# Kernel optimization log

Hardware: AMD Instinct MI355X
Metric: run time of the kernel (lower is better)

## Reference

```python
import jax, jax.numpy as jnp
import numpy as np

B, T, C = 4, 4096, 512


def setup_inputs() -> dict:
    key = jax.random.key(0)
    ks = jax.random.split(key, 7)
    s = 1.0 / np.sqrt(C)  # ~ torch Linear init scale
    X = jax.random.normal(ks[0], (B, T, C), jnp.float32)
    S_n = jnp.zeros((B, C, C), jnp.float32)
    W_Q = jax.random.normal(ks[1], (C, C), jnp.float32) * s
    b_Q = jax.random.normal(ks[2], (C,), jnp.float32) * s
    W_K = jax.random.normal(ks[3], (C, C), jnp.float32) * s
    b_K = jax.random.normal(ks[4], (C,), jnp.float32) * s
    W_V = jax.random.normal(ks[5], (C, C), jnp.float32) * s
    b_V = jax.random.normal(ks[6], (C,), jnp.float32) * s
    return {"X": X, "S_n": S_n, "W_Q": W_Q, "b_Q": b_Q,
            "W_K": W_K, "b_K": b_K, "W_V": W_V, "b_V": b_V}


def reference(X, S_n, W_Q, b_Q, W_K, b_K, W_V, b_V):
    # forward_chunkwise with chunk_len = 1 (exact simplification):
    #   per step t (gamma g_t from linspace(0.96, 0.99, T)):
    #     inner_t = (q_t . k_t) * v_t            # D = gamma^0 = 1
    #     cross_t = (q_t @ S) * g_t              # e[:,0,:] = g^1
    #     O_t     = tanh(inner_t + cross_t)
    #     S      <- k_t^T v_t + g_t * S          # D[-1] = 1, g**chunk_len = g
    Bx, Tx, Cx = X.shape
    Q = X @ W_Q + b_Q  # [B,T,C]
    K = X @ W_K + b_K
    V = X @ W_V + b_V
    gammas = jnp.linspace(0.96, 0.99, Tx).astype(X.dtype)

    def step(S, inp):
        q, k, v, g = inp  # q,k,v: [B,C]; g: scalar
        inner = jnp.sum(q * k, axis=-1, keepdims=True) * v      # [B,C]
        cross = jnp.einsum('bc,bcd->bd', q, S) * g              # [B,C]
        O = jnp.tanh(inner + cross)
        S_new = jnp.einsum('bc,bd->bcd', k, v) + S * g          # [B,C,C]
        return S_new, O

    # original resets S_n to zeros regardless of the passed-in value
    S0 = jnp.zeros_like(S_n)
    S_final, O = jax.lax.scan(
        step, S0,
        (Q.transpose(1, 0, 2), K.transpose(1, 0, 2), V.transpose(1, 0, 2), gammas))
    out = O.transpose(1, 0, 2)  # [B,T,C]
    return out, S_final
```

## Files before the change

### kernel.cpp

```cpp
#include <hip/hip_runtime.h>
#include <math.h>

#define Bsz  4
#define Tlen 4096
#define Cdim 512
#define CUT  (-12.0f)
#define NBE  8388608

typedef unsigned int u32;
typedef _Float16 f16;
typedef __attribute__((ext_vector_type(8))) _Float16 f16x8;
typedef __attribute__((ext_vector_type(4))) float floatx4;
#define MFMA_F16(a,b,c) __builtin_amdgcn_mfma_f32_16x16x32_f16((a),(b),(c),0,0,0)

union pun8 { uint4 u; f16x8 f; };

__device__ __forceinline__ u32 pack2(f16 a, f16 b) {
    return (u32)__builtin_bit_cast(unsigned short, a) |
           ((u32)__builtin_bit_cast(unsigned short, b) << 16);
}
__device__ __forceinline__ u32 splitpack(float v) {
    f16 h = (f16)v;
    f16 l = (f16)(v - (float)h);
    return pack2(h, l);
}
__device__ __forceinline__ void unpack8(const u32* p, f16x8& h, f16x8& l) {
    uint4 q0 = *(const uint4*)p;
    uint4 q1 = *(const uint4*)(p + 4);
    pun8 ph, pl;
    ph.u.x = __builtin_amdgcn_perm(q0.y, q0.x, 0x05040100u);
    pl.u.x = __builtin_amdgcn_perm(q0.y, q0.x, 0x07060302u);
    ph.u.y = __builtin_amdgcn_perm(q0.w, q0.z, 0x05040100u);
    pl.u.y = __builtin_amdgcn_perm(q0.w, q0.z, 0x07060302u);
    ph.u.z = __builtin_amdgcn_perm(q1.y, q1.x, 0x05040100u);
    pl.u.z = __builtin_amdgcn_perm(q1.y, q1.x, 0x07060302u);
    ph.u.w = __builtin_amdgcn_perm(q1.w, q1.z, 0x05040100u);
    pl.u.w = __builtin_amdgcn_perm(q1.w, q1.z, 0x07060302u);
    h = ph.f; l = pl.f;
}
__device__ __forceinline__ float tanh_fast(float x) {
    return 1.0f - 2.0f / (__expf(2.0f * x) + 1.0f);
}

__global__ __launch_bounds__(256) void prep_kernel(
    const float* __restrict__ X,
    const float* __restrict__ WQ, const float* __restrict__ WK,
    const float* __restrict__ WV,
    f16* __restrict__ Xf, f16* __restrict__ WT,
    float* __restrict__ Lg, float* __restrict__ Wfin, int* __restrict__ sLo) {
    __shared__ char pshm[18432];
    int bid = blockIdx.x, tid = threadIdx.x;
    if (bid < 2048) {
        size_t i = ((size_t)bid * 256 + tid) * 16;
        float v[16];
#pragma unroll
        for (int j = 0; j < 4; ++j) {
            float4 a = *(const float4*)(X + i + j * 4);
            v[j*4+0]=a.x; v[j*4+1]=a.y; v[j*4+2]=a.z; v[j*4+3]=a.w;
        }
        uint4 o0, o1;
        o0.x = pack2((f16)v[0], (f16)v[1]);   o0.y = pack2((f16)v[2], (f16)v[3]);
        o0.z = pack2((f16)v[4], (f16)v[5]);   o0.w = pack2((f16)v[6], (f16)v[7]);
        o1.x = pack2((f16)v[8], (f16)v[9]);   o1.y = pack2((f16)v[10], (f16)v[11]);
        o1.z = pack2((f16)v[12], (f16)v[13]); o1.w = pack2((f16)v[14], (f16)v[15]);
        *(uint4*)(Xf + i) = o0;
        *(uint4*)(Xf + i + 8) = o1;
    } else if (bid < 2240) {
        f16* tile = (f16*)pshm;
        int wb = bid - 2048;
        int mat = wb >> 6, rem = wb & 63;
        int k0 = (rem >> 3) * 64, n0 = (rem & 7) * 64;
        const float* W = (mat == 0) ? WQ : (mat == 1) ? WK : WV;
        int row = tid >> 2, q = tid & 3;
        const float* src = W + (size_t)(k0 + row) * Cdim + n0 + q * 16;
        float vv[16];
#pragma unroll
        for (int j = 0; j < 4; ++j) {
            float4 v = *(const float4*)(src + j * 4);
            vv[j*4+0]=v.x; vv[j*4+1]=v.y; vv[j*4+2]=v.z; vv[j*4+3]=v.w;
        }
#pragma unroll
        for (int j = 0; j < 16; ++j) tile[(q * 16 + j) * 72 + row] = (f16)vv[j];
        __syncthreads();
        f16x8 r0 = *(const f16x8*)(tile + row * 72 + q * 16);
        f16x8 r1 = *(const f16x8*)(tile + row * 72 + q * 16 + 8);
        f16* dst = WT + ((size_t)mat * Cdim + n0 + row) * Cdim + k0 + q * 16;
        *(f16x8*)dst = r0;
        *(f16x8*)(dst + 8) = r1;
    } else {
        float* Lsh = (float*)pshm;
        float* sums = (float*)(pshm + 16400);
        float lg[16];
        float local = 0.f;
        int base = tid * 16;
#pragma unroll
        for (int i = 0; i < 16; ++i) {
            int t = base + i;
            float g = 0.96f + 0.03f * ((float)t * (1.0f / 4095.0f));
            lg[i] = logf(g);
            local += lg[i];
        }
        sums[tid] = local;
        __syncthreads();
        for (int off = 1; off < 256; off <<= 1) {
            float v = sums[tid];
            if (tid >= off) v += sums[tid - off];
            __syncthreads();
            sums[tid] = v;
            __syncthreads();
        }
        float pre = (tid == 0) ? 0.f : sums[tid - 1];
#pragma unroll
        for (int i = 0; i < 16; ++i) {
            Lsh[base + i] = pre;
            pre += lg[i];
        }
        if (tid == 255) Lsh[4096] = pre;
        __syncthreads();
        for (int t = tid; t < 4097; t += 256) Lg[t] = Lsh[t];
        float LT = Lsh[4096];
        for (int s = tid; s < 4096; s += 256) Wfin[s] = __expf(LT - Lsh[s + 1]);
        if (tid < 64) {
            float ref = Lsh[tid * 64 + 1];
            int st_hi = tid >> 1;
            int lo = st_hi;
            for (int st = 0; st < st_hi; ++st)
                if (ref - Lsh[st * 128 + 128] > CUT) { lo = st; break; }
            sLo[tid] = lo;
        }
    }
}

__global__ __launch_bounds__(256, 2) void qkv_mfma(
    const f16* __restrict__ Xf, const f16* __restrict__ WT,
    const float* __restrict__ bQ, const float* __restrict__ bK,
    const float* __restrict__ bV,
    f16* __restrict__ Qf, f16* __restrict__ Kf,
    f16* __restrict__ KT, f16* __restrict__ VT) {
    __shared__ char smem[34816];
    u32* sX = (u32*)smem;
    u32* sW = (u32*)(smem + 16384);
    f16* sB = (f16*)smem;

    int tid = threadIdx.x, lane = tid & 63, wid = tid >> 6;
    int l16 = lane & 15, quad = lane >> 4;
    int wm = wid & 1, wn = wid >> 1;
    int xb = blockIdx.x;
    int mat = xb >> 2, n0 = (xb & 3) * 128;
    int m0 = blockIdx.y * 128;

    floatx4 acc[4][4];
#pragma unroll
    for (int i = 0; i < 4; ++i)
#pragma unroll
        for (int j = 0; j < 4; ++j) acc[i][j] = (floatx4)0.f;

    int srow = tid >> 1, shalf = tid & 1;
    int arow_a = wm * 64 + l16, arow_b = wn * 64 + l16;
    int swz_f = (l16 & 7) << 2;

    for (int kc = 0; kc < Cdim; kc += 64) {
        __syncthreads();
        {
            const f16* gx = Xf + (size_t)(m0 + srow) * Cdim + kc + shalf * 32;
            const f16* gw = WT + ((size_t)(mat * Cdim) + n0 + srow) * Cdim + kc + shalf * 32;
            int wswz = (srow & 7) << 2;
#pragma unroll
            for (int k = 0; k < 4; ++k) {
                uint4 xv = *(const uint4*)(gx + k * 8);
                uint4 wv = *(const uint4*)(gw + k * 8);
                int w = shalf * 16 + k * 4;
                *(uint4*)&sX[srow * 32 + (w ^ wswz)] = xv;
                *(uint4*)&sW[srow * 32 + (w ^ wswz)] = wv;
            }
        }
        __syncthreads();
#pragma unroll
        for (int ks = 0; ks < 2; ++ks) {
            int w0 = ks * 16 + quad * 4;
            f16x8 af[4], bf[4];
#pragma unroll
            for (int mt = 0; mt < 4; ++mt)
                af[mt] = ((pun8*)&sX[(arow_a + mt * 16) * 32 + (w0 ^ swz_f)])->f;
#pragma unroll
            for (int nt = 0; nt < 4; ++nt)
                bf[nt] = ((pun8*)&sW[(arow_b + nt * 16) * 32 + (w0 ^ swz_f)])->f;
#pragma unroll
            for (int mt = 0; mt < 4; ++mt)
#pragma unroll
                for (int nt = 0; nt < 4; ++nt)
                    acc[mt][nt] = MFMA_F16(af[mt], bf[nt], acc[mt][nt]);
        }
    }

    const float* bias = (mat == 0) ? bQ : (mat == 1) ? bK : bV;
    float bv[4];
#pragma unroll
    for (int nt = 0; nt < 4; ++nt) bv[nt] = bias[n0 + wn * 64 + nt * 16 + l16];
    float cv[4][4][4];
#pragma unroll
    for (int mt = 0; mt < 4; ++mt)
#pragma unroll
        for (int nt = 0; nt < 4; ++nt)
#pragma unroll
            for (int r = 0; r < 4; ++r) cv[mt][nt][r] = acc[mt][nt][r] + bv[nt];

    int b = m0 >> 12, tloc = m0 & 4095;

    if (mat == 2) {
#pragma unroll
        for (int mt = 0; mt < 4; ++mt)
#pragma unroll
            for (int nt = 0; nt < 4; ++nt) {
                int d = n0 + wn * 64 + nt * 16 + l16;
                int t = tloc + wm * 64 + mt * 16 + quad * 4;
                uint2 w;
                w.x = pack2((f16)cv[mt][nt][0], (f16)cv[mt][nt][1]);
                w.y = pack2((f16)cv[mt][nt][2], (f16)cv[mt][nt][3]);
                *(uint2*)(VT + ((size_t)(b * Cdim + d)) * Tlen + t) = w;
            }
    } else {
        if (mat == 1) {
#pragma unroll
            for (int mt = 0; mt < 4; ++mt)
#pragma unroll
                for (int nt = 0; nt < 4; ++nt) {
                    int d = n0 + wn * 64 + nt * 16 + l16;
                    int t = tloc + wm * 64 + mt * 16 + quad * 4;
                    uint2 w;
                    w.x = pack2((f16)cv[mt][nt][0], (f16)cv[mt][nt][1]);
                    w.y = pack2((f16)cv[mt][nt][2], (f16)cv[mt][nt][3]);
                    *(uint2*)(KT + ((size_t)(b * Cdim + d)) * Tlen + t) = w;
                }
        }
        __syncthreads();
#pragma unroll
        for (int mt = 0; mt < 4; ++mt)
#pragma unroll
            for (int nt = 0; nt < 4; ++nt)
#pragma unroll
                for (int r = 0; r < 4; ++r)
                    sB[(wm * 64 + mt * 16 + quad * 4 + r) * 136 +
                       wn * 64 + nt * 16 + l16] = (f16)cv[mt][nt][r];
        __syncthreads();
        {
            f16* Out = (mat == 0) ? Qf : Kf;
            int r2 = tid >> 1, h2 = tid & 1;
            f16* dst = Out + (size_t)(m0 + r2) * Cdim + n0 + h2 * 64;
#pragma unroll
            for (int j = 0; j < 8; ++j)
                *(uint4*)(dst + j * 8) = *(const uint4*)(sB + r2 * 136 + h2 * 64 + j * 8);
        }
    }
}

__global__ __launch_bounds__(512, 2) void attn_mfma(
    const f16* __restrict__ Qf, const f16* __restrict__ Kf,
    const f16* __restrict__ VT, const float* __restrict__ Lg,
    const int* __restrict__ sLo, float* __restrict__ out) {
    __shared__ char smem[99328];
    u32* sQ  = (u32*)smem;
    u32* sPc = (u32*)(smem + 65536);

    int tid = threadIdx.x, lane = tid & 63, wid = tid >> 6;
    int l16 = lane & 15, quad = lane >> 4;
    int mw = wid & 1;
    int nw = wid >> 1;

    int x = blockIdx.x & 7, j = blockIdx.x >> 3;
    int b = x >> 1;
    int tt = (j << 1) | (x & 1);
    int t0 = tt * 64;
    size_t bT = (size_t)b * Tlen;
    int lo = sLo[tt], hi = tt >> 1;

    {
        int r = tid >> 3, c8 = tid & 7;
        const f16* src = Qf + (bT + t0 + r) * Cdim + c8 * 64;
        int wswz = (r & 7) << 2;
#pragma unroll
        for (int k = 0; k < 8; ++k) {
            uint4 v = *(const uint4*)(src + k * 8);
            int w = c8 * 32 + k * 4;
            *(uint4*)&sQ[r * 256 + (w ^ wswz)] = v;
        }
    }

    float aT[2][4];
#pragma unroll
    for (int mt = 0; mt < 2; ++mt)
#pragma unroll
        for (int r = 0; r < 4; ++r)
            aT[mt][r] = Lg[t0 + mw * 32 + mt * 16 + quad * 4 + r + 1];

    floatx4 oacc[2][8];
#pragma unroll
    for (int i = 0; i < 2; ++i)
#pragma unroll
        for (int jj = 0; jj < 8; ++jj) oacc[i][jj] = (floatx4)0.f;

    int swz_f = (l16 & 7) << 2;
    int rowA0 = (mw * 32 + l16) * 256;
    int rowA1 = (mw * 32 + 16 + l16) * 256;

    __syncthreads();

    for (int st = lo; st <= hi; ++st) {
        int s0 = st * 128;
        float lsp[2];
#pragma unroll
        for (int sq = 0; sq < 2; ++sq)
            lsp[sq] = Lg[s0 + nw * 32 + sq * 16 + l16 + 1];

        floatx4 pacc[2][2];
#pragma unroll
        for (int i = 0; i < 2; ++i)
#pragma unroll
            for (int jj = 0; jj < 2; ++jj) pacc[i][jj] = (floatx4)0.f;

        const f16* kb = Kf + (bT + s0 + nw * 32 + l16) * Cdim;
#pragma unroll 4
        for (int kc = 0; kc < 16; ++kc) {
            int ko = kc * 32 + quad * 8;
            int w0 = kc * 16 + quad * 4;
            f16x8 a0 = ((pun8*)&sQ[rowA0 + (w0 ^ swz_f)])->f;
            f16x8 a1 = ((pun8*)&sQ[rowA1 + (w0 ^ swz_f)])->f;
            f16x8 b0 = *(const f16x8*)(kb + ko);
            f16x8 b1 = *(const f16x8*)(kb + 16 * Cdim + ko);
            pacc[0][0] = MFMA_F16(a0, b0, pacc[0][0]);
            pacc[0][1] = MFMA_F16(a0, b1, pacc[0][1]);
            pacc[1][0] = MFMA_F16(a1, b0, pacc[1][0]);
            pacc[1][1] = MFMA_F16(a1, b1, pacc[1][1]);
        }

        __syncthreads();
#pragma unroll
        for (int mt = 0; mt < 2; ++mt)
#pragma unroll
            for (int sq = 0; sq < 2; ++sq)
#pragma unroll
                for (int r = 0; r < 4; ++r) {
                    int tl = mw * 32 + mt * 16 + quad * 4 + r;
                    int sl = nw * 32 + sq * 16 + l16;
                    int t = t0 + tl, s = s0 + sl;
                    float p = pacc[mt][sq][r];
                    p = (s <= t) ? p * __expf(aT[mt][r] - lsp[sq]) : 0.f;
                    sPc[tl * 132 + (sl ^ ((tl & 7) << 4))] = splitpack(p);
                }
        __syncthreads();

        const f16* vb = VT + ((size_t)(b * Cdim + nw * 128 + l16)) * Tlen + s0;
#pragma unroll
        for (int kf = 0; kf < 4; ++kf) {
            int sb = kf * 32 + quad * 8;
            f16x8 ph[2], pl[2];
#pragma unroll
            for (int mt = 0; mt < 2; ++mt) {
                int tl = mw * 32 + mt * 16 + l16;
                unpack8(&sPc[tl * 132 + (sb ^ ((tl & 7) << 4))], ph[mt], pl[mt]);
            }
#pragma unroll
            for (int nt = 0; nt < 8; ++nt) {
                f16x8 vf = *(const f16x8*)(vb + (size_t)nt * 16 * Tlen + sb);
#pragma unroll
                for (int mt = 0; mt < 2; ++mt) {
                    oacc[mt][nt] = MFMA_F16(ph[mt], vf, oacc[mt][nt]);
                    oacc[mt][nt] = MFMA_F16(pl[mt], vf, oacc[mt][nt]);
                }
            }
        }
    }

#pragma unroll
    for (int mt = 0; mt < 2; ++mt)
#pragma unroll
        for (int nt = 0; nt < 8; ++nt)
#pragma unroll
            for (int r = 0; r < 4; ++r) {
                int t = t0 + mw * 32 + mt * 16 + quad * 4 + r;
                int d = nw * 128 + nt * 16 + l16;
                out[(bT + t) * (size_t)Cdim + d] = tanh_fast(oacc[mt][nt][r]);
            }
}

__global__ __launch_bounds__(256) void sfinal_mfma(
    const f16* __restrict__ KT, const f16* __restrict__ VT,
    const float* __restrict__ Lg, const float* __restrict__ Wfin,
    float* __restrict__ S) {
    __shared__ f16 sA[64 * 72];
    __shared__ f16 sB2[64 * 72];
    int tid = threadIdx.x, lane = tid & 63, wid = tid >> 6;
    int l16 = lane & 15, quad = lane >> 4;
    int wv_c = wid & 1, wv_d = wid >> 1;
    int c0 = blockIdx.x * 64, d0 = blockIdx.y * 64, b = blockIdx.z;
    float LT = Lg[Tlen];
    floatx4 acc[2][2];
#pragma unroll
    for (int i = 0; i < 2; ++i)
#pragma unroll
        for (int jj = 0; jj < 2; ++jj) acc[i][jj] = (floatx4)0.f;

    int s0start = Tlen - 64;
    for (int s0 = 0; s0 < Tlen; s0 += 64)
        if (LT - Lg[s0 + 64] > CUT) { s0start = s0; break; }

    int row = tid >> 2, q = tid & 3;
    for (int s0 = s0start; s0 < Tlen; s0 += 64) {
        __syncthreads();
        {
            const f16* g = KT + ((size_t)(b * Cdim + c0 + row)) * Tlen + s0 + q * 16;
            f16x8 u0 = *(const f16x8*)g;
            f16x8 u1 = *(const f16x8*)(g + 8);
            float wv[16];
#pragma unroll
            for (int jj = 0; jj < 4; ++jj) {
                float4 w4 = *(const float4*)(Wfin + s0 + q * 16 + jj * 4);
                wv[jj*4+0]=w4.x; wv[jj*4+1]=w4.y; wv[jj*4+2]=w4.z; wv[jj*4+3]=w4.w;
            }
            f16x8 o0, o1;
#pragma unroll
            for (int jj = 0; jj < 8; ++jj) o0[jj] = (f16)((float)u0[jj] * wv[jj]);
#pragma unroll
            for (int jj = 0; jj < 8; ++jj) o1[jj] = (f16)((float)u1[jj] * wv[8 + jj]);
            *(f16x8*)(sA + row * 72 + q * 16) = o0;
            *(f16x8*)(sA + row * 72 + q * 16 + 8) = o1;
            const f16* gv = VT + ((size_t)(b * Cdim + d0 + row)) * Tlen + s0 + q * 16;
            uint4 v0 = *(const uint4*)gv, v1 = *(const uint4*)(gv + 8);
            *(uint4*)(sB2 + row * 72 + q * 16) = v0;
            *(uint4*)(sB2 + row * 72 + q * 16 + 8) = v1;
        }
        __syncthreads();
#pragma unroll
        for (int ks = 0; ks < 2; ++ks) {
            int ko = ks * 32 + quad * 8;
            f16x8 a0 = *(const f16x8*)(sA + (wv_c * 32 + l16) * 72 + ko);
            f16x8 a1 = *(const f16x8*)(sA + (wv_c * 32 + 16 + l16) * 72 + ko);
            f16x8 b0 = *(const f16x8*)(sB2 + (wv_d * 32 + l16) * 72 + ko);
            f16x8 b1 = *(const f16x8*)(sB2 + (wv_d * 32 + 16 + l16) * 72 + ko);
            acc[0][0] = MFMA_F16(a0, b0, acc[0][0]);
            acc[0][1] = MFMA_F16(a0, b1, acc[0][1]);
            acc[1][0] = MFMA_F16(a1, b0, acc[1][0]);
            acc[1][1] = MFMA_F16(a1, b1, acc[1][1]);
        }
    }
#pragma unroll
    for (int ct = 0; ct < 2; ++ct)
#pragma unroll
        for (int dt = 0; dt < 2; ++dt)
#pragma unroll
            for (int r = 0; r < 4; ++r) {
                int c = c0 + wv_c * 32 + ct * 16 + quad * 4 + r;
                int d = d0 + wv_d * 32 + dt * 16 + l16;
                S[((size_t)(b * Cdim + c)) * Cdim + d] = acc[ct][dt][r];
            }
}

extern "C" void kernel_launch(void* const* d_in, const int* in_sizes, int n_in,
                              void* d_out, int out_size, void* d_ws, size_t ws_size,
                              hipStream_t stream) {
    (void)in_sizes; (void)n_in; (void)out_size; (void)ws_size;
    const float* X  = (const float*)d_in[0];
    const float* WQ = (const float*)d_in[2];
    const float* bQ = (const float*)d_in[3];
    const float* WK = (const float*)d_in[4];
    const float* bK = (const float*)d_in[5];
    const float* WV = (const float*)d_in[6];
    const float* bV = (const float*)d_in[7];

    float* out   = (float*)d_out;
    float* S_out = out + (size_t)NBE;

    char* ws = (char*)d_ws;
    f16*   Xf   = (f16*)(ws);
    f16*   Qf   = (f16*)(ws + 2ull * NBE);
    f16*   Kf   = (f16*)(ws + 4ull * NBE);
    f16*   KT   = (f16*)(ws + 6ull * NBE);
    f16*   VT   = (f16*)(ws + 8ull * NBE);
    f16*   WT   = (f16*)(ws + 10ull * NBE);
    char*  tail = ws + 10ull * NBE + (2u << 20);
    float* Lg   = (float*)(tail);
    float* Wfin = (float*)(tail + 16512);
    int*   sLo  = (int*)(tail + 16512 + 16384);

    prep_kernel<<<2241, 256, 0, stream>>>(X, WQ, WK, WV, Xf, WT, Lg, Wfin, sLo);
    qkv_mfma<<<dim3(12, 128), 256, 0, stream>>>(Xf, WT, bQ, bK, bV, Qf, Kf, KT, VT);
    attn_mfma<<<256, 512, 0, stream>>>(Qf, Kf, VT, Lg, sLo, out);
    sfinal_mfma<<<dim3(8, 8, Bsz), 256, 0, stream>>>(KT, VT, Lg, Wfin, S_out);
}
```

Before: 304.8 us.

## Halve attention query tile to 32 rows and reorder blocks for load balance

The chunked attention kernel now processes 32 query rows per block instead of 64. Each of the 8 waves owns a 16-key slice of the score tile and a 64-column slice of the output. This doubles the grid to 512 blocks, halves shared memory so 4 blocks can share a CU, and updates the sLo window table to 32-row granularity. Block indices are permuted so long (late) and short (early) tiles are interleaved, spreading the causal triangle more evenly across CUs. In exchange, each block reuses its K and V tiles over fewer query rows, which raises global traffic per unit of work.

```diff
diff --git a/kernel.cpp b/kernel.cpp
--- a/kernel.cpp
+++ b/kernel.cpp
@@ -120,9 +120,9 @@
         for (int t = tid; t < 4097; t += 256) Lg[t] = Lsh[t];
         float LT = Lsh[4096];
         for (int s = tid; s < 4096; s += 256) Wfin[s] = __expf(LT - Lsh[s + 1]);
-        if (tid < 64) {
-            float ref = Lsh[tid * 64 + 1];
-            int st_hi = tid >> 1;
+        if (tid < 128) {
+            float ref = Lsh[tid * 32 + 1];
+            int st_hi = tid >> 2;
             int lo = st_hi;
             for (int st = 0; st < st_hi; ++st)
                 if (ref - Lsh[st * 128 + 128] > CUT) { lo = st; break; }
@@ -254,34 +254,34 @@
     }
 }
 
-__global__ __launch_bounds__(512, 2) void attn_mfma(
+__global__ __launch_bounds__(512, 4) void attn_mfma(
     const f16* __restrict__ Qf, const f16* __restrict__ Kf,
     const f16* __restrict__ VT, const float* __restrict__ Lg,
     const int* __restrict__ sLo, float* __restrict__ out) {
-    __shared__ char smem[99328];
+    __shared__ char smem[49664];
     u32* sQ  = (u32*)smem;
-    u32* sPc = (u32*)(smem + 65536);
+    u32* sPc = (u32*)(smem + 32768);
 
     int tid = threadIdx.x, lane = tid & 63, wid = tid >> 6;
     int l16 = lane & 15, quad = lane >> 4;
-    int mw = wid & 1;
-    int nw = wid >> 1;
-
-    int x = blockIdx.x & 7, j = blockIdx.x >> 3;
-    int b = x >> 1;
-    int tt = (j << 1) | (x & 1);
-    int t0 = tt * 64;
+
+    int i = blockIdx.x;
+    int halfsel = i >> 8, q = i & 255;
+    int L = ((q & 7) << 5) | (q >> 3);
+    int b = L >> 6, ttl = L & 63;
+    int tt = halfsel ? (63 - ttl) : (64 + ttl);
+    int t0 = tt * 32;
     size_t bT = (size_t)b * Tlen;
-    int lo = sLo[tt], hi = tt >> 1;
+    int lo = sLo[tt], hi = tt >> 2;
 
     {
-        int r = tid >> 3, c8 = tid & 7;
-        const f16* src = Qf + (bT + t0 + r) * Cdim + c8 * 64;
+        int r = tid >> 4, c16 = tid & 15;
+        const f16* src = Qf + (bT + t0 + r) * Cdim + c16 * 32;
         int wswz = (r & 7) << 2;
 #pragma unroll
-        for (int k = 0; k < 8; ++k) {
+        for (int k = 0; k < 4; ++k) {
             uint4 v = *(const uint4*)(src + k * 8);
-            int w = c8 * 32 + k * 4;
+            int w = c16 * 16 + k * 4;
             *(uint4*)&sQ[r * 256 + (w ^ wswz)] = v;
         }
     }
@@ -291,76 +291,65 @@
     for (int mt = 0; mt < 2; ++mt)
 #pragma unroll
         for (int r = 0; r < 4; ++r)
-            aT[mt][r] = Lg[t0 + mw * 32 + mt * 16 + quad * 4 + r + 1];
-
-    floatx4 oacc[2][8];
-#pragma unroll
-    for (int i = 0; i < 2; ++i)
-#pragma unroll
-        for (int jj = 0; jj < 8; ++jj) oacc[i][jj] = (floatx4)0.f;
+            aT[mt][r] = Lg[t0 + mt * 16 + quad * 4 + r + 1];
+
+    floatx4 oacc[2][4];
+#pragma unroll
+    for (int mt = 0; mt < 2; ++mt)
+#pragma unroll
+        for (int nt = 0; nt < 4; ++nt) oacc[mt][nt] = (floatx4)0.f;
 
     int swz_f = (l16 & 7) << 2;
-    int rowA0 = (mw * 32 + l16) * 256;
-    int rowA1 = (mw * 32 + 16 + l16) * 256;
+    int rowA0 = l16 * 256;
+    int rowA1 = (16 + l16) * 256;
 
     __syncthreads();
 
     for (int st = lo; st <= hi; ++st) {
         int s0 = st * 128;
-        float lsp[2];
-#pragma unroll
-        for (int sq = 0; sq < 2; ++sq)
-            lsp[sq] = Lg[s0 + nw * 32 + sq * 16 + l16 + 1];
-
-        floatx4 pacc[2][2];
-#pragma unroll
-        for (int i = 0; i < 2; ++i)
-#pragma unroll
-            for (int jj = 0; jj < 2; ++jj) pacc[i][jj] = (floatx4)0.f;
-
-        const f16* kb = Kf + (bT + s0 + nw * 32 + l16) * Cdim;
+        float lsp = Lg[s0 + wid * 16 + l16 + 1];
+
+        floatx4 pacc[2];
+        pacc[0] = (floatx4)0.f; pacc[1] = (floatx4)0.f;
+
+        const f16* kb = Kf + (bT + s0 + wid * 16 + l16) * Cdim;
 #pragma unroll 4
         for (int kc = 0; kc < 16; ++kc) {
             int ko = kc * 32 + quad * 8;
             int w0 = kc * 16 + quad * 4;
             f16x8 a0 = ((pun8*)&sQ[rowA0 + (w0 ^ swz_f)])->f;
             f16x8 a1 = ((pun8*)&sQ[rowA1 + (w0 ^ swz_f)])->f;
-            f16x8 b0 = *(const f16x8*)(kb + ko);
-            f16x8 b1 = *(const f16x8*)(kb + 16 * Cdim + ko);
-            pacc[0][0] = MFMA_F16(a0, b0, pacc[0][0]);
-            pacc[0][1] = MFMA_F16(a0, b1, pacc[0][1]);
-            pacc[1][0] = MFMA_F16(a1, b0, pacc[1][0]);
-            pacc[1][1] = MFMA_F16(a1, b1, pacc[1][1]);
+            f16x8 bk = *(const f16x8*)(kb + ko);
+            pacc[0] = MFMA_F16(a0, bk, pacc[0]);
+            pacc[1] = MFMA_F16(a1, bk, pacc[1]);
         }
 
         __syncthreads();
 #pragma unroll
         for (int mt = 0; mt < 2; ++mt)
 #pragma unroll
-            for (int sq = 0; sq < 2; ++sq)
-#pragma unroll
-                for (int r = 0; r < 4; ++r) {
-                    int tl = mw * 32 + mt * 16 + quad * 4 + r;
-                    int sl = nw * 32 + sq * 16 + l16;
-                    int t = t0 + tl, s = s0 + sl;
-                    float p = pacc[mt][sq][r];
-                    p = (s <= t) ? p * __expf(aT[mt][r] - lsp[sq]) : 0.f;
-                    sPc[tl * 132 + (sl ^ ((tl & 7) << 4))] = splitpack(p);
-                }
-        __syncthreads();
-
-        const f16* vb = VT + ((size_t)(b * Cdim + nw * 128 + l16)) * Tlen + s0;
+            for (int r = 0; r < 4; ++r) {
+                int tl = mt * 16 + quad * 4 + r;
+                int sl = wid * 16 + l16;
+                int t = t0 + tl, s = s0 + sl;
+                float p = pacc[mt][r];
+                p = (s <= t) ? p * __expf(aT[mt][r] - lsp) : 0.f;
+                sPc[tl * 132 + (sl ^ ((tl & 7) << 4))] = splitpack(p);
+            }
+        __syncthreads();
+
+        const f16* vb = VT + ((size_t)(b * Cdim + wid * 64 + l16)) * Tlen + s0;
 #pragma unroll
         for (int kf = 0; kf < 4; ++kf) {
             int sb = kf * 32 + quad * 8;
             f16x8 ph[2], pl[2];
 #pragma unroll
             for (int mt = 0; mt < 2; ++mt) {
-                int tl = mw * 32 + mt * 16 + l16;
+                int tl = mt * 16 + l16;
                 unpack8(&sPc[tl * 132 + (sb ^ ((tl & 7) << 4))], ph[mt], pl[mt]);
             }
 #pragma unroll
-            for (int nt = 0; nt < 8; ++nt) {
+            for (int nt = 0; nt < 4; ++nt) {
                 f16x8 vf = *(const f16x8*)(vb + (size_t)nt * 16 * Tlen + sb);
 #pragma unroll
                 for (int mt = 0; mt < 2; ++mt) {
@@ -374,11 +363,11 @@
 #pragma unroll
     for (int mt = 0; mt < 2; ++mt)
 #pragma unroll
-        for (int nt = 0; nt < 8; ++nt)
+        for (int nt = 0; nt < 4; ++nt)
 #pragma unroll
             for (int r = 0; r < 4; ++r) {
-                int t = t0 + mw * 32 + mt * 16 + quad * 4 + r;
-                int d = nw * 128 + nt * 16 + l16;
+                int t = t0 + mt * 16 + quad * 4 + r;
+                int d = wid * 64 + nt * 16 + l16;
                 out[(bT + t) * (size_t)Cdim + d] = tanh_fast(oacc[mt][nt][r]);
             }
 }
@@ -484,6 +473,6 @@
 
     prep_kernel<<<2241, 256, 0, stream>>>(X, WQ, WK, WV, Xf, WT, Lg, Wfin, sLo);
     qkv_mfma<<<dim3(12, 128), 256, 0, stream>>>(Xf, WT, bQ, bK, bV, Qf, Kf, KT, VT);
-    attn_mfma<<<256, 512, 0, stream>>>(Qf, Kf, VT, Lg, sLo, out);
+    attn_mfma<<<512, 512, 0, stream>>>(Qf, Kf, VT, Lg, sLo, out);
     sfinal_mfma<<<dim3(8, 8, Bsz), 256, 0, stream>>>(KT, VT, Lg, Wfin, S_out);
 }
```

Result: faster. 260.0 us (-14.7%).
